# Optimization experiments

Hardware: AMD Instinct MI355X
Metric: run time of the kernel (lower is better)

Reference implementation:

```python
import jax
import jax.numpy as jnp
import numpy as np
from jax import lax

B = 256
H = W = 64
N_ACTIONS = 18
N_EXPERTS = 8
HIDDEN = 1024
LATENT = 256
EXPERT_DIM = 512
TOP_K = 2
CONV_OUT = 64 * H * W  # padding=1, k=3 convs preserve HxW


def setup_inputs() -> dict:
    key = jax.random.key(0)
    ks = jax.random.split(key, 18)

    def rn(k, shape, fan_in):
        # kaiming-ish scale, keeps activations sane
        return jax.random.normal(k, shape, jnp.float32) * np.float32(np.sqrt(2.0 / fan_in))

    return {
        "pixel_obs": jax.random.normal(ks[0], (B, 1, H, W), jnp.float32),
        # conv weights in torch OIHW layout
        "conv1_w": rn(ks[1], (16, 1, 3, 3), 9),
        "conv1_b": jnp.zeros((16,), jnp.float32),
        "conv2_w": rn(ks[2], (32, 16, 3, 3), 16 * 9),
        "conv2_b": jnp.zeros((32,), jnp.float32),
        "conv3_w": rn(ks[3], (64, 32, 3, 3), 32 * 9),
        "conv3_b": jnp.zeros((64,), jnp.float32),
        # linear weights stored [in, out]
        "fc1_w": rn(ks[4], (CONV_OUT, HIDDEN), CONV_OUT),
        "fc1_b": jnp.zeros((HIDDEN,), jnp.float32),
        "fc2_w": rn(ks[5], (HIDDEN, LATENT), HIDDEN),
        "fc2_b": jnp.zeros((LATENT,), jnp.float32),
        "gate_w": rn(ks[6], (LATENT, N_EXPERTS), LATENT),
        "gate_b": jnp.zeros((N_EXPERTS,), jnp.float32),
        # all experts stacked: [E, in, out]
        "exp_w1": rn(ks[7], (N_EXPERTS, LATENT, EXPERT_DIM), LATENT),
        "exp_b1": jnp.zeros((N_EXPERTS, EXPERT_DIM), jnp.float32),
        "exp_w2": rn(ks[8], (N_EXPERTS, EXPERT_DIM, N_ACTIONS), EXPERT_DIM),
        "exp_b2": jnp.zeros((N_EXPERTS, N_ACTIONS), jnp.float32),
    }


def _conv(x, w, b):
    y = lax.conv_general_dilated(
        x, w, window_strides=(1, 1), padding="SAME",
        dimension_numbers=("NCHW", "OIHW", "NCHW"))
    return jax.nn.relu(y + b[None, :, None, None])


def reference(pixel_obs, conv1_w, conv1_b, conv2_w, conv2_b, conv3_w, conv3_b,
              fc1_w, fc1_b, fc2_w, fc2_b, gate_w, gate_b,
              exp_w1, exp_b1, exp_w2, exp_b2):
    h = _conv(pixel_obs, conv1_w, conv1_b)
    h = _conv(h, conv2_w, conv2_b)
    h = _conv(h, conv3_w, conv3_b)          # [B, 64, H, W]
    flat = h.reshape(h.shape[0], -1)         # NCHW flatten matches torch .view
    s = jax.nn.relu(flat @ fc1_w + fc1_b)
    s = jax.nn.relu(s @ fc2_w + fc2_b)       # shared features [B, LATENT]

    gate_probs = jax.nn.softmax(s @ gate_w + gate_b, axis=1)  # [B, E]
    top_v, top_i = lax.top_k(gate_probs, TOP_K)               # [B, K]
    top_v = top_v / jnp.sum(top_v, axis=1, keepdims=True)

    # dense per-expert compute, as in the original (all experts on all tokens)
    eh = jax.nn.relu(jnp.einsum("bl,elh->beh", s, exp_w1) + exp_b1[None])
    eo = jnp.einsum("beh,eha->bea", eh, exp_w2) + exp_b2[None]  # [B, E, A]

    # fused gather + weighted combine (replaces the python double loop)
    sel = jnp.take_along_axis(eo, top_i[:, :, None], axis=1)    # [B, K, A]
    action_logits = jnp.sum(top_v[:, :, None] * sel, axis=1)    # [B, A]
    return action_logits, gate_probs
```

## Files before the change

### kernel.cpp

```cpp
#include <hip/hip_runtime.h>

typedef _Float16 f16x8 __attribute__((ext_vector_type(8)));
typedef short    s16x8 __attribute__((ext_vector_type(8)));
typedef float    f32x4 __attribute__((ext_vector_type(4)));

__device__ __forceinline__ unsigned short f2bf(float f) {
  union { float f; unsigned u; } x; x.f = f;
  unsigned r = (x.u + 0x7fffu + ((x.u >> 16) & 1u)) >> 16;
  return (unsigned short)r;
}
__device__ __forceinline__ float bf2f(unsigned short u) {
  union { unsigned u; float f; } x; x.u = ((unsigned)u) << 16; return x.f;
}
__device__ __forceinline__ unsigned short f2h_bits(float f) {
  union { _Float16 h; unsigned short u; } c; c.h = (_Float16)f; return c.u;
}

__global__ void prepack_w(const float* __restrict__ w, _Float16* __restrict__ ph,
                          _Float16* __restrict__ pl, int COUT, int CIN, int KPAD)
{
  const int idx = blockIdx.x * 256 + threadIdx.x;
  const int KTOT = 3 * KPAD;
  if (idx >= COUT * KTOT) return;
  const int oc = idx / KTOT;
  const int rem = idx - oc * KTOT;
  const int y = rem / KPAD;
  const int kk = rem - y * KPAD;
  float v = 0.f;
  if (kk < 3 * CIN) {
    const int tx = kk / CIN;
    const int ic = kk - tx * CIN;
    v = w[((size_t)oc * CIN + ic) * 9 + y * 3 + tx];
  }
  const _Float16 h = (_Float16)v;
  ph[idx] = h;
  pl[idx] = (_Float16)((v - (float)h) * 2048.0f);
}

__global__ __launch_bounds__(256)
void conv1_k(const float* __restrict__ obs, const float* __restrict__ w,
             const float* __restrict__ bias, _Float16* __restrict__ outh,
             _Float16* __restrict__ outl)
{
  const int rg = blockIdx.x;
  const int b = blockIdx.y;
  const int tid = threadIdx.x;
  const int lr = tid >> 6;
  const int col = tid & 63;
  __shared__ float xs[6][66];
  __shared__ float wb[9][16];
  for (int idx = tid; idx < 6 * 66; idx += 256) {
    const int r = idx / 66, c = idx - (idx / 66) * 66;
    const int gr = rg * 4 - 1 + r, gc = c - 1;
    xs[r][c] = (gr >= 0 && gr < 64 && gc >= 0 && gc < 64)
                   ? obs[(size_t)b * 4096 + gr * 64 + gc] : 0.f;
  }
  if (tid < 144) wb[tid / 16][tid & 15] = w[(tid & 15) * 9 + tid / 16];
  __syncthreads();
  float acc[16];
#pragma unroll
  for (int o = 0; o < 16; ++o) acc[o] = bias[o];
#pragma unroll
  for (int ty = 0; ty < 3; ++ty)
#pragma unroll
    for (int tx = 0; tx < 3; ++tx) {
      const float x = xs[lr + ty][col + tx];
#pragma unroll
      for (int o = 0; o < 16; ++o) acc[o] = fmaf(x, wb[ty * 3 + tx][o], acc[o]);
    }
  const size_t base = ((size_t)(b * 64 + rg * 4 + lr) * 64 + col) * 16;
#pragma unroll
  for (int o = 0; o < 16; ++o) {
    const float v = fmaxf(acc[o], 0.f);
    const _Float16 h = (_Float16)v;
    outh[base + o] = h;
    outl[base + o] = (_Float16)((v - (float)h) * 2048.0f);
  }
}

template<int CIN, int COUT, bool NCHW_OUT>
__global__ __launch_bounds__(256)
void conv_mfma(const _Float16* __restrict__ inh, const _Float16* __restrict__ inl,
               const _Float16* __restrict__ wph, const _Float16* __restrict__ wpl,
               const float* __restrict__ bias,
               unsigned short* __restrict__ outh, unsigned short* __restrict__ outl)
{
  constexpr int KFX = (3 * CIN + 31) / 32;
  constexpr int KPAD = KFX * 32;
  constexpr int KTOT = 3 * KPAD;
  constexpr int CP = CIN + 8;
  constexpr int NF = COUT / 32;
  constexpr int STO = NCHW_OUT ? COUT : 1;
  constexpr int STP = NCHW_OUT ? 136 : 8;
  const int rp = blockIdx.x;
  const int b  = blockIdx.y;
  const int r0 = rp * 2;
  const int tid = threadIdx.x;
  const int lane = tid & 63;
  const int wid = tid >> 6;
  const int wm = wid >> 1;
  const int wn = wid & 1;

  __shared__ _Float16 xh[4][68][CP];
  __shared__ _Float16 xl[4][68][CP];
  __shared__ unsigned short st_h[STO][STP];
  __shared__ unsigned short st_l[STO][STP];

  constexpr int CH = CIN / 8;
  for (int idx = tid; idx < 4 * 68 * CH; idx += 256) {
    const int r = idx / (68 * CH);
    const int rem = idx - r * 68 * CH;
    const int hc = rem / CH;
    const int ch = rem - hc * CH;
    const int gr = r0 - 1 + r;
    const int gc = hc - 1;
    uint4 vh = {0, 0, 0, 0}, vl = {0, 0, 0, 0};
    if (gr >= 0 && gr < 64 && gc >= 0 && gc < 64) {
      const size_t base = ((size_t)(b * 64 + gr) * 64 + gc) * CIN + ch * 8;
      vh = *(const uint4*)(inh + base);
      vl = *(const uint4*)(inl + base);
    }
    *(uint4*)&xh[r][hc][ch * 8] = vh;
    *(uint4*)&xl[r][hc][ch * 8] = vl;
  }
  __syncthreads();

  f32x4 accm[4][NF];
  f32x4 accc[4][NF];
#pragma unroll
  for (int mf = 0; mf < 4; ++mf)
#pragma unroll
    for (int nf = 0; nf < NF; ++nf) { accm[mf][nf] = {}; accc[mf][nf] = {}; }

  const int lm = lane & 15;
  const int ch8 = (lane >> 4) * 8;

#pragma unroll
  for (int kf = 0; kf < 3 * KFX; ++kf) {
    const int y = kf / KFX;
    const int fx = kf - y * KFX;
    const int kk = fx * 32 + ch8;
    f16x8 bh[NF], bl[NF];
#pragma unroll
    for (int nf = 0; nf < NF; ++nf) {
      const int oc = wn * (16 * NF) + nf * 16 + lm;
      bh[nf] = *(const f16x8*)(wph + (size_t)oc * KTOT + kf * 32 + ch8);
      bl[nf] = *(const f16x8*)(wpl + (size_t)oc * KTOT + kf * 32 + ch8);
    }
#pragma unroll
    for (int mf = 0; mf < 4; ++mf) {
      const int col = mf * 16 + lm;
      const f16x8 ah = *(const f16x8*)&xh[wm + y][col + kk / CIN][kk % CIN];
      const f16x8 al = *(const f16x8*)&xl[wm + y][col + kk / CIN][kk % CIN];
#pragma unroll
      for (int nf = 0; nf < NF; ++nf) {
        accm[mf][nf] = __builtin_amdgcn_mfma_f32_16x16x32_f16(ah, bh[nf], accm[mf][nf], 0, 0, 0);
        accc[mf][nf] = __builtin_amdgcn_mfma_f32_16x16x32_f16(ah, bl[nf], accc[mf][nf], 0, 0, 0);
        accc[mf][nf] = __builtin_amdgcn_mfma_f32_16x16x32_f16(al, bh[nf], accc[mf][nf], 0, 0, 0);
      }
    }
  }

  if constexpr (NCHW_OUT) {
#pragma unroll
    for (int nf = 0; nf < NF; ++nf) {
      const int oc = wn * (16 * NF) + nf * 16 + lm;
      const float bv = bias[oc];
#pragma unroll
      for (int mf = 0; mf < 4; ++mf) {
        unsigned short hv[4], lv[4];
#pragma unroll
        for (int r = 0; r < 4; ++r) {
          const float v = fmaxf(accm[mf][nf][r] + accc[mf][nf][r] * (1.0f / 2048.0f) + bv, 0.f);
          const unsigned short hb = f2bf(v);
          hv[r] = hb;
          lv[r] = f2bf(v - bf2f(hb));
        }
        const int px = wm * 64 + mf * 16 + (lane >> 4) * 4;
        *(ushort4*)&st_h[oc][px] = make_ushort4(hv[0], hv[1], hv[2], hv[3]);
        *(ushort4*)&st_l[oc][px] = make_ushort4(lv[0], lv[1], lv[2], lv[3]);
      }
    }
    __syncthreads();
    const int oc2 = tid >> 2;
    const int seg = tid & 3;
    const size_t gb = ((size_t)b * COUT + oc2) * 4096 + r0 * 64 + seg * 32;
#pragma unroll
    for (int j2 = 0; j2 < 4; ++j2) {
      *(uint4*)(outh + gb + j2 * 8) = *(const uint4*)&st_h[oc2][seg * 32 + j2 * 8];
      *(uint4*)(outl + gb + j2 * 8) = *(const uint4*)&st_l[oc2][seg * 32 + j2 * 8];
    }
  } else {
    const int orow = r0 + wm;
#pragma unroll
    for (int nf = 0; nf < NF; ++nf) {
      const int oc = wn * (16 * NF) + nf * 16 + lm;
      const float bv = bias[oc];
#pragma unroll
      for (int mf = 0; mf < 4; ++mf) {
#pragma unroll
        for (int r = 0; r < 4; ++r) {
          const int x = mf * 16 + (lane >> 4) * 4 + r;
          const float v = fmaxf(accm[mf][nf][r] + accc[mf][nf][r] * (1.0f / 2048.0f) + bv, 0.f);
          const _Float16 h = (_Float16)v;
          const size_t oi = ((size_t)(b * 64 + orow) * 64 + x) * COUT + oc;
          outh[oi] = f2h_bits(v) , outh[oi] = ({ union { _Float16 f; unsigned short u; } c; c.f = h; c.u; });
          outl[oi] = ({ union { _Float16 f; unsigned short u; } c; c.f = (_Float16)((v - (float)h) * 2048.0f); c.u; });
        }
      }
    }
  }
}

__global__ __launch_bounds__(512, 2)
void fc1_gemm_v11(const unsigned short* __restrict__ Ahi, const unsigned short* __restrict__ Alo,
                  const float* __restrict__ W, float* __restrict__ P)
{
  const int sk = blockIdx.x;
  const int nt = blockIdx.y;
  const int nc0 = nt * 256;
  const int tid = threadIdx.x;
  const int lane = tid & 63;
  const int wid = tid >> 6;
  const int wm = wid >> 1;
  const int wn = wid & 1;

  __shared__ unsigned short Ah[2][256][32];
  __shared__ unsigned short Al[2][256][32];
  __shared__ unsigned short Bh[2][256][32];
  __shared__ unsigned short Bl[2][256][32];

  f32x4 acc[4][8] = {};

  const int nl = tid & 255;
  const int kq = tid >> 8;
  const int q = lane >> 4;

  const size_t kbase = (size_t)sk * 4096;
  constexpr int NIT = 128;

  const int Rbase = wid * 32;
  const int lrow0 = Rbase + (lane >> 2);
  const int lrow1 = Rbase + 16 + (lane >> 2);
  const int sd = lane & 3;
  const int ssrc0 = sd ^ ((lrow0 >> 1) & 3);
  const int ssrc1 = sd ^ ((lrow1 >> 1) & 3);
  const size_t goff0 = (size_t)lrow0 * 262144 + ssrc0 * 8;
  const size_t goff1 = (size_t)lrow1 * 262144 + ssrc1 * 8;

#define ISSUE_A(p, k0)                                                                     \
  {                                                                                        \
    __builtin_amdgcn_global_load_lds(                                                      \
        (const __attribute__((address_space(1))) unsigned int*)(Ahi + goff0 + (k0)),       \
        (__attribute__((address_space(3))) unsigned int*)&Ah[p][Rbase][0], 16, 0, 0);      \
    __builtin_amdgcn_global_load_lds(                                                      \
        (const __attribute__((address_space(1))) unsigned int*)(Ahi + goff1 + (k0)),       \
        (__attribute__((address_space(3))) unsigned int*)&Ah[p][Rbase + 16][0], 16, 0, 0); \
    __builtin_amdgcn_global_load_lds(                                                      \
        (const __attribute__((address_space(1))) unsigned int*)(Alo + goff0 + (k0)),       \
        (__attribute__((address_space(3))) unsigned int*)&Al[p][Rbase][0], 16, 0, 0);      \
    __builtin_amdgcn_global_load_lds(                                                      \
        (const __attribute__((address_space(1))) unsigned int*)(Alo + goff1 + (k0)),       \
        (__attribute__((address_space(3))) unsigned int*)&Al[p][Rbase + 16][0], 16, 0, 0); \
  }

#define LOAD_W(k0, wr)                                                      \
  {                                                                         \
    const size_t jb = (k0) + kq * 16;                                       \
    _Pragma("unroll") for (int i = 0; i < 16; ++i) {                        \
      wr[i] = W[(jb + i) * 1024 + nc0 + nl];                                \
    }                                                                       \
  }

#define WRITE_B(p, wr)                                                      \
  {                                                                         \
    _Pragma("unroll") for (int h2 = 0; h2 < 2; ++h2) {                      \
      s16x8 hv, lv;                                                         \
      _Pragma("unroll") for (int j = 0; j < 8; ++j) {                       \
        const float f = wr[h2 * 8 + j];                                     \
        const unsigned short hb = f2bf(f);                                  \
        hv[j] = (short)hb;                                                  \
        lv[j] = (short)f2bf(f - bf2f(hb));                                  \
      }                                                                     \
      const int sw = (kq * 2 + h2) ^ ((nl >> 1) & 3);                       \
      *(s16x8*)&Bh[p][nl][sw * 8] = hv;                                     \
      *(s16x8*)&Bl[p][nl][sw * 8] = lv;                                     \
    }                                                                       \
  }

#define COMPUTE(p)                                                                          \
  {                                                                                         \
    s16x8 ah[4], al[4];                                                                     \
    _Pragma("unroll") for (int mf = 0; mf < 4; ++mf) {                                      \
      const int r = wm * 64 + mf * 16 + (lane & 15);                                        \
      const int s = (q ^ ((r >> 1) & 3)) * 8;                                               \
      ah[mf] = *(const s16x8*)&Ah[p][r][s];                                                 \
      al[mf] = *(const s16x8*)&Al[p][r][s];                                                 \
    }                                                                                       \
    _Pragma("unroll") for (int hf = 0; hf < 2; ++hf) {                                      \
      s16x8 bh[4], bl[4];                                                                   \
      _Pragma("unroll") for (int nf = 0; nf < 4; ++nf) {                                    \
        const int n = wn * 128 + (hf * 4 + nf) * 16 + (lane & 15);                          \
        const int s = (q ^ ((n >> 1) & 3)) * 8;                                             \
        bh[nf] = *(const s16x8*)&Bh[p][n][s];                                               \
        bl[nf] = *(const s16x8*)&Bl[p][n][s];                                               \
      }                                                                                     \
      __builtin_amdgcn_s_setprio(1);                                                        \
      _Pragma("unroll") for (int mf = 0; mf < 4; ++mf)                                      \
        _Pragma("unroll") for (int nf = 0; nf < 4; ++nf) {                                  \
          acc[mf][hf*4+nf] = __builtin_amdgcn_mfma_f32_16x16x32_bf16(ah[mf], bh[nf], acc[mf][hf*4+nf], 0, 0, 0); \
          acc[mf][hf*4+nf] = __builtin_amdgcn_mfma_f32_16x16x32_bf16(al[mf], bh[nf], acc[mf][hf*4+nf], 0, 0, 0); \
          acc[mf][hf*4+nf] = __builtin_amdgcn_mfma_f32_16x16x32_bf16(ah[mf], bl[nf], acc[mf][hf*4+nf], 0, 0, 0); \
        }                                                                                   \
      __builtin_amdgcn_s_setprio(0);                                                        \
    }                                                                                       \
  }

  {
    float wr[16];
    LOAD_W(kbase, wr);
    ISSUE_A(0, kbase);
    WRITE_B(0, wr);
    LOAD_W(kbase + 32, wr);
    ISSUE_A(1, kbase + 32);
    asm volatile("s_waitcnt vmcnt(20)\n\ts_waitcnt lgkmcnt(0)\n\ts_barrier" ::: "memory");
  }

  {
    float wr[16];
    LOAD_W(kbase + 32, wr);
    for (int it = 0; it < NIT - 1; ++it) {
      const int cur = it & 1;
      COMPUTE(cur);
      WRITE_B(cur ^ 1, wr);
      asm volatile("s_waitcnt vmcnt(0)\n\ts_waitcnt lgkmcnt(0)\n\ts_barrier" ::: "memory");
      if (it + 2 < NIT) {
        const size_t k2 = kbase + (size_t)(it + 2) * 32;
        LOAD_W(k2, wr);
        ISSUE_A(cur, k2);
      }
    }
    COMPUTE((NIT - 1) & 1);
  }
#undef ISSUE_A
#undef LOAD_W
#undef WRITE_B
#undef COMPUTE

#pragma unroll
  for (int mf = 0; mf < 4; ++mf) {
    const int rbase = wm * 64 + mf * 16 + ((lane >> 4) << 2);
#pragma unroll
    for (int nf = 0; nf < 8; ++nf) {
      const int c = nc0 + wn * 128 + nf * 16 + (lane & 15);
#pragma unroll
      for (int r = 0; r < 4; ++r)
        P[((size_t)sk * 256 + rbase + r) * 1024 + c] = acc[mf][nf][r];
    }
  }
}

__global__ __launch_bounds__(256)
void fc1_reduce(const float* __restrict__ P, const float* __restrict__ bias,
                float* __restrict__ s1)
{
  const int idx = blockIdx.x * 256 + threadIdx.x;
  const int n = idx & 1023;
  float a = bias[n];
#pragma unroll 8
  for (int sk = 0; sk < 64; ++sk) a += P[(size_t)sk * 262144 + idx];
  s1[idx] = fmaxf(a, 0.f);
}

__global__ __launch_bounds__(256)
void fc2_k(const float* __restrict__ s1, const float* __restrict__ w,
           const float* __restrict__ b, float* __restrict__ s2)
{
  const int bb = blockIdx.x;
  const int t = threadIdx.x;
  __shared__ float xr[1024];
  for (int i = t; i < 1024; i += 256) xr[i] = s1[bb * 1024 + i];
  __syncthreads();
  float a0 = b[t], a1 = 0.f, a2 = 0.f, a3 = 0.f;
#pragma unroll 4
  for (int k = 0; k < 1024; k += 4) {
    a0 += xr[k + 0] * w[(k + 0) * 256 + t];
    a1 += xr[k + 1] * w[(k + 1) * 256 + t];
    a2 += xr[k + 2] * w[(k + 2) * 256 + t];
    a3 += xr[k + 3] * w[(k + 3) * 256 + t];
  }
  s2[bb * 256 + t] = fmaxf(a0 + a1 + a2 + a3, 0.f);
}

__global__ __launch_bounds__(64)
void gate_k(const float* __restrict__ s2, const float* __restrict__ gw,
            const float* __restrict__ gb, float* __restrict__ gate_out,
            int* __restrict__ topi, float* __restrict__ topv)
{
  const int bb = blockIdx.x;
  const int l = threadIdx.x;
  float part[8] = {};
  for (int k = l; k < 256; k += 64) {
    const float x = s2[bb * 256 + k];
#pragma unroll
    for (int e = 0; e < 8; ++e) part[e] += x * gw[k * 8 + e];
  }
#pragma unroll
  for (int off = 32; off > 0; off >>= 1)
#pragma unroll
    for (int e = 0; e < 8; ++e) part[e] += __shfl_down(part[e], off);

  if (l == 0) {
    float lg[8];
    float m = -1e30f;
#pragma unroll
    for (int e = 0; e < 8; ++e) { lg[e] = part[e] + gb[e]; m = fmaxf(m, lg[e]); }
    float s = 0.f;
    float p[8];
#pragma unroll
    for (int e = 0; e < 8; ++e) { p[e] = expf(lg[e] - m); s += p[e]; }
#pragma unroll
    for (int e = 0; e < 8; ++e) { p[e] = p[e] / s; gate_out[bb * 8 + e] = p[e]; }
    int i0 = 0;
#pragma unroll
    for (int e = 1; e < 8; ++e) if (p[e] > p[i0]) i0 = e;
    int i1 = (i0 == 0) ? 1 : 0;
#pragma unroll
    for (int e = 0; e < 8; ++e) if (e != i0 && p[e] > p[i1]) i1 = e;
    const float v0 = p[i0], v1 = p[i1];
    topi[bb * 2 + 0] = i0; topi[bb * 2 + 1] = i1;
    topv[bb * 2 + 0] = v0 / (v0 + v1); topv[bb * 2 + 1] = v1 / (v0 + v1);
  }
}

__global__ __launch_bounds__(256)
void expert_k(const float* __restrict__ s2, const float* __restrict__ w1,
              const float* __restrict__ b1, const float* __restrict__ w2,
              const float* __restrict__ b2, const int* __restrict__ topi,
              const float* __restrict__ topv, float* __restrict__ out)
{
  const int bb = blockIdx.x;
  const int t = threadIdx.x;
  __shared__ float xr[256];
  __shared__ float eh[512];
  __shared__ float partial[18][8];
  xr[t] = s2[bb * 256 + t];
  float logit = 0.f;
  for (int kk = 0; kk < 2; ++kk) {
    __syncthreads();
    const int e = topi[bb * 2 + kk];
    const float tv = topv[bb * 2 + kk];
    const float* W1 = w1 + (size_t)e * 256 * 512;
    float a0 = b1[e * 512 + t], a1 = b1[e * 512 + 256 + t];
#pragma unroll 4
    for (int k = 0; k < 256; ++k) {
      const float x = xr[k];
      a0 = fmaf(x, W1[k * 512 + t], a0);
      a1 = fmaf(x, W1[k * 512 + 256 + t], a1);
    }
    eh[t] = fmaxf(a0, 0.f);
    eh[256 + t] = fmaxf(a1, 0.f);
    __syncthreads();
    if (t < 144) {
      const int a = t >> 3, q2 = t & 7;
      const float* W2 = w2 + (size_t)e * 512 * 18;
      float pp = 0.f;
      for (int h = q2 * 64; h < q2 * 64 + 64; ++h) pp = fmaf(eh[h], W2[h * 18 + a], pp);
      partial[a][q2] = pp;
    }
    __syncthreads();
    if (t < 18) {
      float s = b2[e * 18 + t];
#pragma unroll
      for (int q2 = 0; q2 < 8; ++q2) s += partial[t][q2];
      logit = fmaf(tv, s, logit);
    }
  }
  if (t < 18) out[bb * 18 + t] = logit;
}

extern "C" void kernel_launch(void* const* d_in, const int* in_sizes, int n_in,
                              void* d_out, int out_size, void* d_ws, size_t ws_size,
                              hipStream_t stream) {
  const float* obs     = (const float*)d_in[0];
  const float* conv1_w = (const float*)d_in[1];
  const float* conv1_b = (const float*)d_in[2];
  const float* conv2_w = (const float*)d_in[3];
  const float* conv2_b = (const float*)d_in[4];
  const float* conv3_w = (const float*)d_in[5];
  const float* conv3_b = (const float*)d_in[6];
  const float* fc1_w   = (const float*)d_in[7];
  const float* fc1_b   = (const float*)d_in[8];
  const float* fc2_w   = (const float*)d_in[9];
  const float* fc2_b   = (const float*)d_in[10];
  const float* gate_w  = (const float*)d_in[11];
  const float* gate_b  = (const float*)d_in[12];
  const float* exp_w1  = (const float*)d_in[13];
  const float* exp_b1  = (const float*)d_in[14];
  const float* exp_w2  = (const float*)d_in[15];
  const float* exp_b2  = (const float*)d_in[16];

  char* ws = (char*)d_ws;
  const size_t MB = 1ull << 20;
  const size_t KB = 1ull << 10;
  _Float16*       act1h = (_Float16*)(ws);
  _Float16*       act1l = (_Float16*)(ws + 32 * MB);
  _Float16*       act2h = (_Float16*)(ws + 64 * MB);
  _Float16*       act2l = (_Float16*)(ws + 128 * MB);
  unsigned short* act3h = (unsigned short*)(ws + 192 * MB);
  unsigned short* act3l = (unsigned short*)(ws + 320 * MB);
  float*    P     = (float*)(ws);
  _Float16* wp2h  = (_Float16*)(ws + 448 * MB);
  _Float16* wp2l  = (_Float16*)(ws + 448 * MB + 64 * KB);
  _Float16* wp3h  = (_Float16*)(ws + 448 * MB + 128 * KB);
  _Float16* wp3l  = (_Float16*)(ws + 448 * MB + 192 * KB);
  float*    s2    = (float*)(ws + 448 * MB + 256 * KB);
  int*      topi  = (int*)(ws + 448 * MB + 512 * KB);
  float*    topv  = (float*)(ws + 448 * MB + 516 * KB);
  float*    s1    = (float*)(ws + 449 * MB);
  float*    out   = (float*)d_out;

  prepack_w<<<(32 * 192 + 255) / 256, 256, 0, stream>>>(conv2_w, wp2h, wp2l, 32, 16, 64);
  prepack_w<<<(64 * 288 + 255) / 256, 256, 0, stream>>>(conv3_w, wp3h, wp3l, 64, 32, 96);

  conv1_k<<<dim3(16, 256), 256, 0, stream>>>(obs, conv1_w, conv1_b, act1h, act1l);
  conv_mfma<16, 32, false><<<dim3(32, 256), 256, 0, stream>>>(act1h, act1l, wp2h, wp2l, conv2_b,
                                                              (unsigned short*)act2h, (unsigned short*)act2l);
  conv_mfma<32, 64, true ><<<dim3(32, 256), 256, 0, stream>>>(act2h, act2l, wp3h, wp3l, conv3_b,
                                                              act3h, act3l);

  fc1_gemm_v11<<<dim3(64, 4), 512, 0, stream>>>(act3h, act3l, fc1_w, P);
  fc1_reduce<<<1024, 256, 0, stream>>>(P, fc1_b, s1);
  fc2_k<<<256, 256, 0, stream>>>(s1, fc2_w, fc2_b, s2);
  gate_k<<<256, 64, 0, stream>>>(s2, gate_w, gate_b, out + 256 * 18, topi, topv);
  expert_k<<<256, 256, 0, stream>>>(s2, exp_w1, exp_b1, exp_w2, exp_b2, topi, topv, out);
}
```

Before: 894.3 us.

## Restructure fc1 GEMM main loop to interleave LDS reads, global loads and MFMAs

The fc1 split-K GEMM loop is restructured so each iteration reads A and the first half of B from LDS, issues the first half of the MFMAs while the second B half is read, and issues the next global loads plus the B write into the other buffer between the two MFMA halves. It uses two register buffers for W rows, manually unrolled by two. The goal is to hide global-load and LDS latency behind MFMA work instead of waiting on a full vmcnt(0) barrier per iteration. It adds extra barriers per iteration and more register pressure. The conv epilogue store is also cleaned up to drop a redundant store.

```diff
diff --git a/kernel.cpp b/kernel.cpp
--- a/kernel.cpp
+++ b/kernel.cpp
@@ -11,9 +11,6 @@
 }
 __device__ __forceinline__ float bf2f(unsigned short u) {
   union { unsigned u; float f; } x; x.u = ((unsigned)u) << 16; return x.f;
-}
-__device__ __forceinline__ unsigned short f2h_bits(float f) {
-  union { _Float16 h; unsigned short u; } c; c.h = (_Float16)f; return c.u;
 }
 
 __global__ void prepack_w(const float* __restrict__ w, _Float16* __restrict__ ph,
@@ -203,9 +200,12 @@
           const int x = mf * 16 + (lane >> 4) * 4 + r;
           const float v = fmaxf(accm[mf][nf][r] + accc[mf][nf][r] * (1.0f / 2048.0f) + bv, 0.f);
           const _Float16 h = (_Float16)v;
+          union { _Float16 f; unsigned short u; } ch_, cl_;
+          ch_.f = h;
+          cl_.f = (_Float16)((v - (float)h) * 2048.0f);
           const size_t oi = ((size_t)(b * 64 + orow) * 64 + x) * COUT + oc;
-          outh[oi] = f2h_bits(v) , outh[oi] = ({ union { _Float16 f; unsigned short u; } c; c.f = h; c.u; });
-          outl[oi] = ({ union { _Float16 f; unsigned short u; } c; c.f = (_Float16)((v - (float)h) * 2048.0f); c.u; });
+          outh[oi] = ch_.u;
+          outl[oi] = cl_.u;
         }
       }
     }
@@ -213,7 +213,7 @@
 }
 
 __global__ __launch_bounds__(512, 2)
-void fc1_gemm_v11(const unsigned short* __restrict__ Ahi, const unsigned short* __restrict__ Alo,
+void fc1_gemm_v13(const unsigned short* __restrict__ Ahi, const unsigned short* __restrict__ Alo,
                   const float* __restrict__ W, float* __restrict__ P)
 {
   const int sk = blockIdx.x;
@@ -288,64 +288,71 @@
     }                                                                       \
   }
 
-#define COMPUTE(p)                                                                          \
-  {                                                                                         \
-    s16x8 ah[4], al[4];                                                                     \
-    _Pragma("unroll") for (int mf = 0; mf < 4; ++mf) {                                      \
-      const int r = wm * 64 + mf * 16 + (lane & 15);                                        \
-      const int s = (q ^ ((r >> 1) & 3)) * 8;                                               \
-      ah[mf] = *(const s16x8*)&Ah[p][r][s];                                                 \
-      al[mf] = *(const s16x8*)&Al[p][r][s];                                                 \
-    }                                                                                       \
-    _Pragma("unroll") for (int hf = 0; hf < 2; ++hf) {                                      \
-      s16x8 bh[4], bl[4];                                                                   \
-      _Pragma("unroll") for (int nf = 0; nf < 4; ++nf) {                                    \
-        const int n = wn * 128 + (hf * 4 + nf) * 16 + (lane & 15);                          \
-        const int s = (q ^ ((n >> 1) & 3)) * 8;                                             \
-        bh[nf] = *(const s16x8*)&Bh[p][n][s];                                               \
-        bl[nf] = *(const s16x8*)&Bl[p][n][s];                                               \
-      }                                                                                     \
-      __builtin_amdgcn_s_setprio(1);                                                        \
-      _Pragma("unroll") for (int mf = 0; mf < 4; ++mf)                                      \
-        _Pragma("unroll") for (int nf = 0; nf < 4; ++nf) {                                  \
-          acc[mf][hf*4+nf] = __builtin_amdgcn_mfma_f32_16x16x32_bf16(ah[mf], bh[nf], acc[mf][hf*4+nf], 0, 0, 0); \
-          acc[mf][hf*4+nf] = __builtin_amdgcn_mfma_f32_16x16x32_bf16(al[mf], bh[nf], acc[mf][hf*4+nf], 0, 0, 0); \
-          acc[mf][hf*4+nf] = __builtin_amdgcn_mfma_f32_16x16x32_bf16(ah[mf], bl[nf], acc[mf][hf*4+nf], 0, 0, 0); \
-        }                                                                                   \
-      __builtin_amdgcn_s_setprio(0);                                                        \
-    }                                                                                       \
-  }
-
-  {
-    float wr[16];
-    LOAD_W(kbase, wr);
-    ISSUE_A(0, kbase);
-    WRITE_B(0, wr);
-    LOAD_W(kbase + 32, wr);
-    ISSUE_A(1, kbase + 32);
-    asm volatile("s_waitcnt vmcnt(20)\n\ts_waitcnt lgkmcnt(0)\n\ts_barrier" ::: "memory");
-  }
-
-  {
-    float wr[16];
-    LOAD_W(kbase + 32, wr);
-    for (int it = 0; it < NIT - 1; ++it) {
-      const int cur = it & 1;
-      COMPUTE(cur);
-      WRITE_B(cur ^ 1, wr);
-      asm volatile("s_waitcnt vmcnt(0)\n\ts_waitcnt lgkmcnt(0)\n\ts_barrier" ::: "memory");
-      if (it + 2 < NIT) {
-        const size_t k2 = kbase + (size_t)(it + 2) * 32;
-        LOAD_W(k2, wr);
-        ISSUE_A(cur, k2);
-      }
-    }
-    COMPUTE((NIT - 1) & 1);
+#define READ_A(p, ah, al)                                                   \
+  _Pragma("unroll") for (int mf = 0; mf < 4; ++mf) {                        \
+    const int r = wm * 64 + mf * 16 + (lane & 15);                          \
+    const int s = (q ^ ((r >> 1) & 3)) * 8;                                 \
+    ah[mf] = *(const s16x8*)&Ah[p][r][s];                                   \
+    al[mf] = *(const s16x8*)&Al[p][r][s];                                   \
+  }
+
+#define READ_B(p, hfc, bh, bl)                                              \
+  _Pragma("unroll") for (int nf = 0; nf < 4; ++nf) {                        \
+    const int n = wn * 128 + ((hfc) * 4 + nf) * 16 + (lane & 15);           \
+    const int s = (q ^ ((n >> 1) & 3)) * 8;                                 \
+    bh[nf] = *(const s16x8*)&Bh[p][n][s];                                   \
+    bl[nf] = *(const s16x8*)&Bl[p][n][s];                                   \
+  }
+
+#define MFMA_HF(hfc, ah, al, bh, bl)                                        \
+  __builtin_amdgcn_s_setprio(1);                                            \
+  _Pragma("unroll") for (int mf = 0; mf < 4; ++mf)                          \
+    _Pragma("unroll") for (int nf = 0; nf < 4; ++nf) {                      \
+      acc[mf][(hfc)*4+nf] = __builtin_amdgcn_mfma_f32_16x16x32_bf16(ah[mf], bh[nf], acc[mf][(hfc)*4+nf], 0, 0, 0); \
+      acc[mf][(hfc)*4+nf] = __builtin_amdgcn_mfma_f32_16x16x32_bf16(al[mf], bh[nf], acc[mf][(hfc)*4+nf], 0, 0, 0); \
+      acc[mf][(hfc)*4+nf] = __builtin_amdgcn_mfma_f32_16x16x32_bf16(ah[mf], bl[nf], acc[mf][(hfc)*4+nf], 0, 0, 0); \
+    }                                                                       \
+  __builtin_amdgcn_s_setprio(0);
+
+#define ITER(cur, wrCur, wrNext, it)                                        \
+  {                                                                         \
+    s16x8 ah[4], al[4], bh0[4], bl0[4], bh1[4], bl1[4];                     \
+    READ_A(cur, ah, al);                                                    \
+    READ_B(cur, 0, bh0, bl0);                                               \
+    asm volatile("s_waitcnt lgkmcnt(0)\n\ts_barrier" ::: "memory");         \
+    READ_B(cur, 1, bh1, bl1);                                               \
+    MFMA_HF(0, ah, al, bh0, bl0);                                           \
+    asm volatile("s_waitcnt lgkmcnt(0)\n\ts_barrier" ::: "memory");         \
+    if ((it) + 2 < NIT) {                                                   \
+      const size_t k2 = kbase + (size_t)((it) + 2) * 32;                    \
+      ISSUE_A(cur, k2);                                                     \
+      LOAD_W(k2, wrNext);                                                   \
+    }                                                                       \
+    if ((it) + 1 < NIT) WRITE_B(cur ^ 1, wrCur);                            \
+    MFMA_HF(1, ah, al, bh1, bl1);                                           \
+    asm volatile("s_waitcnt lgkmcnt(0)\n\ts_barrier" ::: "memory");         \
+  }
+
+  float wrA[16], wrB[16];
+
+  LOAD_W(kbase, wrA);
+  ISSUE_A(0, kbase);
+  WRITE_B(0, wrA);
+  ISSUE_A(1, kbase + 32);
+  LOAD_W(kbase + 32, wrA);
+  asm volatile("s_waitcnt vmcnt(20)\n\ts_waitcnt lgkmcnt(0)\n\ts_barrier" ::: "memory");
+
+  for (int it = 0; it < NIT; it += 2) {
+    ITER(0, wrA, wrB, it);
+    ITER(1, wrB, wrA, it + 1);
   }
 #undef ISSUE_A
 #undef LOAD_W
 #undef WRITE_B
-#undef COMPUTE
+#undef READ_A
+#undef READ_B
+#undef MFMA_HF
+#undef ITER
 
 #pragma unroll
   for (int mf = 0; mf < 4; ++mf) {
@@ -529,7 +536,7 @@
   conv_mfma<32, 64, true ><<<dim3(32, 256), 256, 0, stream>>>(act2h, act2l, wp3h, wp3l, conv3_b,
                                                               act3h, act3l);
 
-  fc1_gemm_v11<<<dim3(64, 4), 512, 0, stream>>>(act3h, act3l, fc1_w, P);
+  fc1_gemm_v13<<<dim3(64, 4), 512, 0, stream>>>(act3h, act3l, fc1_w, P);
   fc1_reduce<<<1024, 256, 0, stream>>>(P, fc1_b, s1);
   fc2_k<<<256, 256, 0, stream>>>(s1, fc2_w, fc2_b, s2);
   gate_k<<<256, 64, 0, stream>>>(s2, gate_w, gate_b, out + 256 * 18, topi, topv);
```

Result: slower. 1.515 ms (+69.4%).
